# Kernel optimization log

Hardware: AMD Instinct MI355X
Metric: run time of the kernel (lower is better)

## Reference

```python
import jax, jax.numpy as jnp
import numpy as np

DT = 1e-4  # integration step, matches Model(dt=0.0001)
T = 4_000_000


def setup_inputs() -> dict:
    key = jax.random.key(0)
    ks = jax.random.split(key, 8)
    inputs = jax.random.normal(ks[0], (1, T, 3), dtype=jnp.float32)
    # time column made increasing (as in a real signal record)
    t = jnp.arange(T, dtype=jnp.float32) * DT
    inputs = inputs.at[0, :, 0].set(t)
    # small-scale 2x2 system matrices; A shifted toward -0.5*I so the
    # 4M-step linear recurrence is stable (no overflow over long horizons)
    A = -0.5 * jnp.eye(2, dtype=jnp.float32) + 0.05 * jax.random.normal(ks[1], (2, 2), jnp.float32)
    B = 0.1 * jax.random.normal(ks[2], (2, 2), jnp.float32)
    D = 0.1 * jax.random.normal(ks[3], (2, 2), jnp.float32)
    E = 0.1 * jax.random.normal(ks[4], (2, 2), jnp.float32)
    cov_in = 0.1 * jax.random.normal(ks[5], (2, 2), jnp.float32)
    training_params = jax.random.normal(ks[6], (1, 2), jnp.float32)
    initial_states = jnp.zeros((1, 5), dtype=jnp.float32)
    return {"inputs": inputs, "A": A, "B": B, "D": D, "E": E,
            "cov_in": cov_in, "training_params": training_params,
            "initial_states": initial_states}


def reference(inputs, A, B, D, E, cov_in, training_params, initial_states):
    # Faithful to GRCell.call: cov = cov_in every step (new_cov is discarded),
    # so XiCov / XiCovC / transition matrix are time-invariant constants.
    dt = jnp.float32(DT)
    sqrt2 = jnp.sqrt(jnp.float32(2.0))
    x_signal = jnp.array([1.0, 0.0], dtype=inputs.dtype)
    XiCov = (E - cov_in @ B) / sqrt2                      # (2,2)
    XiCovC = XiCov @ (-sqrt2 * B.T)                       # (2,2)
    Trans = jnp.eye(2, dtype=inputs.dtype) + (A - XiCovC) * dt  # I + (A-XiCovC)dt
    Cout = -sqrt2 * B.T * dt                              # output map, (2,2)
    p0 = training_params[0, 0]
    p1 = training_params[0, 1]
    seq = inputs[0]                                       # [T, 3] = (time, dy1, dy2)

    def step(x, inp):
        t = inp[0]
        dy = inp[1:]
        out = Cout @ x                                    # emitted BEFORE update
        x_new = Trans @ x + XiCov @ dy + (p0 * jnp.cos(p1 * t) * dt) * x_signal
        return x_new, out

    x0 = initial_states[0, :2]
    _, outs = jax.lax.scan(step, x0, seq)                 # outs: [T, 2]
    return outs[None]                                     # [1, T, 2]
```

## Files before the change

kernel.cpp:

```cpp
#include <hip/hip_runtime.h>
#include <math.h>


constexpr int   TN  = 4000000;
constexpr float FDT = 1e-4f;
constexpr int   L   = 64;
constexpr int   K   = TN / L;
constexpr int   BT  = 256;
constexpr int   NB  = (K + BT - 1) / BT;

struct Consts {
  float T00, T01, T10, T11;
  float X00, X01, X10, X11;
  float C00, C01, C10, C11;
  float p0, p1;
};

__device__ inline Consts make_consts(const float* __restrict__ A,
                                     const float* __restrict__ B,
                                     const float* __restrict__ E,
                                     const float* __restrict__ cov,
                                     const float* __restrict__ tp) {
  const float s2 = 1.41421356237309515f;
  Consts c;
  float Xi[2][2];
  for (int i = 0; i < 2; ++i)
    for (int j = 0; j < 2; ++j)
      Xi[i][j] = (E[i*2+j] - (cov[i*2+0]*B[0*2+j] + cov[i*2+1]*B[1*2+j])) / s2;
  float XiC[2][2];
  for (int i = 0; i < 2; ++i)
    for (int j = 0; j < 2; ++j)
      XiC[i][j] = Xi[i][0]*(-s2*B[j*2+0]) + Xi[i][1]*(-s2*B[j*2+1]);
  c.T00 = 1.0f + (A[0] - XiC[0][0]) * FDT;
  c.T01 =        (A[1] - XiC[0][1]) * FDT;
  c.T10 =        (A[2] - XiC[1][0]) * FDT;
  c.T11 = 1.0f + (A[3] - XiC[1][1]) * FDT;
  c.X00 = Xi[0][0]; c.X01 = Xi[0][1]; c.X10 = Xi[1][0]; c.X11 = Xi[1][1];
  c.C00 = -s2 * B[0] * FDT;
  c.C01 = -s2 * B[2] * FDT;
  c.C10 = -s2 * B[1] * FDT;
  c.C11 = -s2 * B[3] * FDT;
  c.p0 = tp[0]; c.p1 = tp[1];
  return c;
}

__device__ inline void step(float& x0, float& x1, float t, float a, float b,
                            const Consts& c) {
  float u0 = fmaf(c.X00, a, fmaf(c.X01, b, c.p0 * __cosf(c.p1 * t) * FDT));
  float u1 = fmaf(c.X10, a, c.X11 * b);
  float n0 = fmaf(c.T00, x0, fmaf(c.T01, x1, u0));
  float n1 = fmaf(c.T10, x0, fmaf(c.T11, x1, u1));
  x0 = n0; x1 = n1;
}

__device__ inline void dsq(double* M) {
  double a = M[0]*M[0] + M[1]*M[2];
  double b = M[0]*M[1] + M[1]*M[3];
  double d = M[2]*M[0] + M[3]*M[2];
  double e = M[2]*M[1] + M[3]*M[3];
  M[0] = a; M[1] = b; M[2] = d; M[3] = e;
}

__device__ inline void pow_table(const Consts& c, double (*Pw)[4], int n) {
  double M[4] = {(double)c.T00, (double)c.T01, (double)c.T10, (double)c.T11};
  for (int s = 0; s < 6; ++s) dsq(M);
  Pw[0][0] = M[0]; Pw[0][1] = M[1]; Pw[0][2] = M[2]; Pw[0][3] = M[3];
  for (int i = 1; i < n; ++i) {
    dsq(M);
    Pw[i][0] = M[0]; Pw[i][1] = M[1]; Pw[i][2] = M[2]; Pw[i][3] = M[3];
  }
}

__global__ void __launch_bounds__(BT)
k1(const float* __restrict__ seq, const float* __restrict__ A,
   const float* __restrict__ B, const float* __restrict__ E,
   const float* __restrict__ cov, const float* __restrict__ tp,
   float* __restrict__ Xe, double* __restrict__ agg) {
  const int tid  = threadIdx.x;
  const int lane = tid & 63;
  const int w    = tid >> 6;
  const int k    = blockIdx.x * BT + tid;
  Consts c = make_consts(A, B, E, cov, tp);

  float x0 = 0.f, x1 = 0.f;
  if (k < K) {
    const float4* p = (const float4*)(seq + (size_t)3 * L * k);
    #pragma unroll 4
    for (int q = 0; q < L / 4; ++q) {
      float4 fa = p[3*q+0], fb = p[3*q+1], fc = p[3*q+2];
      step(x0, x1, fa.x, fa.y, fa.z, c);
      step(x0, x1, fa.w, fb.x, fb.y, c);
      step(x0, x1, fb.z, fb.w, fc.x, c);
      step(x0, x1, fc.y, fc.z, fc.w, c);
    }
  }

  double Pw[7][4];
  pow_table(c, Pw, 7);

  double v0 = (double)x0, v1 = (double)x1;
  #pragma unroll
  for (int s = 0; s < 6; ++s) {
    int st = 1 << s;
    double p0 = __shfl_up(v0, st);
    double p1 = __shfl_up(v1, st);
    if (lane >= st) {
      double n0 = Pw[s][0]*p0 + Pw[s][1]*p1 + v0;
      double n1 = Pw[s][2]*p0 + Pw[s][3]*p1 + v1;
      v0 = n0; v1 = n1;
    }
  }

  __shared__ double wagg[4][2];
  if (lane == 63) { wagg[w][0] = v0; wagg[w][1] = v1; }
  __syncthreads();

  double E0 = 0.0, E1 = 0.0;
  for (int ww = 0; ww < w; ++ww) {
    double n0 = Pw[6][0]*E0 + Pw[6][1]*E1 + wagg[ww][0];
    double n1 = Pw[6][2]*E0 + Pw[6][3]*E1 + wagg[ww][1];
    E0 = n0; E1 = n1;
  }

  double pv0 = __shfl_up(v0, 1);
  double pv1 = __shfl_up(v1, 1);
  if (lane == 0) { pv0 = 0.0; pv1 = 0.0; }

  double M0 = 1.0, M1 = 0.0, M2 = 0.0, M3 = 1.0;
  #pragma unroll
  for (int b = 0; b < 6; ++b) {
    if ((lane >> b) & 1) {
      double a0 = Pw[b][0]*M0 + Pw[b][1]*M2;
      double a1 = Pw[b][0]*M1 + Pw[b][1]*M3;
      double a2 = Pw[b][2]*M0 + Pw[b][3]*M2;
      double a3 = Pw[b][2]*M1 + Pw[b][3]*M3;
      M0 = a0; M1 = a1; M2 = a2; M3 = a3;
    }
  }

  double e0 = M0*E0 + M1*E1 + pv0;
  double e1 = M2*E0 + M3*E1 + pv1;
  if (k < K) {
    Xe[2*k]   = (float)e0;
    Xe[2*k+1] = (float)e1;
  }
  if (tid == BT - 1) {
    agg[2*blockIdx.x]   = Pw[6][0]*E0 + Pw[6][1]*E1 + v0;
    agg[2*blockIdx.x+1] = Pw[6][2]*E0 + Pw[6][3]*E1 + v1;
  }
}

__global__ void __launch_bounds__(BT)
k2(const float* __restrict__ A, const float* __restrict__ B,
   const float* __restrict__ E, const float* __restrict__ cov,
   const float* __restrict__ tp, const float* __restrict__ ini,
   const double* __restrict__ agg, double* __restrict__ Yb) {
  __shared__ double sA[2*NB];
  __shared__ double sY[2*NB];
  for (int i = threadIdx.x; i < 2*NB; i += BT) sA[i] = agg[i];
  __syncthreads();
  if (threadIdx.x == 0) {
    Consts c = make_consts(A, B, E, cov, tp);
    double Q[4] = {(double)c.T00, (double)c.T01, (double)c.T10, (double)c.T11};
    for (int s = 0; s < 14; ++s) dsq(Q);
    double y0 = (double)ini[0], y1 = (double)ini[1];
    for (int b = 0; b < NB; ++b) {
      sY[2*b]   = y0;
      sY[2*b+1] = y1;
      double t0 = Q[0]*y0 + Q[1]*y1 + sA[2*b];
      double t1 = Q[2]*y0 + Q[3]*y1 + sA[2*b+1];
      y0 = t0; y1 = t1;
    }
  }
  __syncthreads();
  for (int i = threadIdx.x; i < 2*NB; i += BT) Yb[i] = sY[i];
}

__global__ void __launch_bounds__(BT)
k3(const float* __restrict__ seq, const float* __restrict__ A,
   const float* __restrict__ B, const float* __restrict__ E,
   const float* __restrict__ cov, const float* __restrict__ tp,
   const float* __restrict__ Xe, const double* __restrict__ Yb,
   float* __restrict__ out) {
  const int tid = threadIdx.x;
  const int k   = blockIdx.x * BT + tid;
  if (k >= K) return;
  Consts c = make_consts(A, B, E, cov, tp);

  double Pw[8][4];
  pow_table(c, Pw, 8);
  double M0 = 1.0, M1 = 0.0, M2 = 0.0, M3 = 1.0;
  #pragma unroll
  for (int b = 0; b < 8; ++b) {
    if ((tid >> b) & 1) {
      double a0 = Pw[b][0]*M0 + Pw[b][1]*M2;
      double a1 = Pw[b][0]*M1 + Pw[b][1]*M3;
      double a2 = Pw[b][2]*M0 + Pw[b][3]*M2;
      double a3 = Pw[b][2]*M1 + Pw[b][3]*M3;
      M0 = a0; M1 = a1; M2 = a2; M3 = a3;
    }
  }
  double y0 = Yb[2*blockIdx.x], y1 = Yb[2*blockIdx.x+1];
  float x0 = (float)(M0*y0 + M1*y1 + (double)Xe[2*k]);
  float x1 = (float)(M2*y0 + M3*y1 + (double)Xe[2*k+1]);

  const float4* p  = (const float4*)(seq + (size_t)3 * L * k);
  float4*       op = (float4*)(out + (size_t)2 * L * k);
  #pragma unroll 4
  for (int q = 0; q < L / 4; ++q) {
    float4 fa = p[3*q+0], fb = p[3*q+1], fc = p[3*q+2];
    float4 oA, oB;
    oA.x = fmaf(c.C00, x0, c.C01 * x1); oA.y = fmaf(c.C10, x0, c.C11 * x1);
    step(x0, x1, fa.x, fa.y, fa.z, c);
    oA.z = fmaf(c.C00, x0, c.C01 * x1); oA.w = fmaf(c.C10, x0, c.C11 * x1);
    step(x0, x1, fa.w, fb.x, fb.y, c);
    oB.x = fmaf(c.C00, x0, c.C01 * x1); oB.y = fmaf(c.C10, x0, c.C11 * x1);
    step(x0, x1, fb.z, fb.w, fc.x, c);
    oB.z = fmaf(c.C00, x0, c.C01 * x1); oB.w = fmaf(c.C10, x0, c.C11 * x1);
    step(x0, x1, fc.y, fc.z, fc.w, c);
    op[2*q]   = oA;
    op[2*q+1] = oB;
  }
}

extern "C" void kernel_launch(void* const* d_in, const int* in_sizes, int n_in,
                              void* d_out, int out_size, void* d_ws, size_t ws_size,
                              hipStream_t stream) {
  const float* seq = (const float*)d_in[0];
  const float* A   = (const float*)d_in[1];
  const float* B   = (const float*)d_in[2];
  const float* E   = (const float*)d_in[4];
  const float* cov = (const float*)d_in[5];
  const float* tp  = (const float*)d_in[6];
  const float* ini = (const float*)d_in[7];
  float* out = (float*)d_out;

  float*  Xe  = (float*)d_ws;
  double* agg = (double*)((char*)d_ws + 500224);
  double* Yb  = agg + 2 * NB;

  k1<<<NB, BT, 0, stream>>>(seq, A, B, E, cov, tp, Xe, agg);
  k2<<<1,  BT, 0, stream>>>(A, B, E, cov, tp, ini, agg, Yb);
  k3<<<NB, BT, 0, stream>>>(seq, A, B, E, cov, tp, Xe, Yb, out);
}
```

Before: 134.3 us.

## Shrink chunk length, stage input/output through LDS, parallelize block-carry scan

Cuts the per-thread chunk from 64 to 16 steps, giving four times as many threads and blocks. Input is loaded with coalesced float4 reads into padded shared memory and outputs are written back through shared memory, replacing strided per-thread global accesses. The serial single-thread carry loop over blocks in k2 is replaced by a parallel wave and block scan using matrix powers. The cost is more launched threads, more double-precision power-table setup per thread, and heavy LDS use that may limit occupancy.

Measured after the change: 127.0 us. -5.5%, faster.

```diff
diff --git a/kernel.cpp b/kernel.cpp
--- a/kernel.cpp
+++ b/kernel.cpp
@@ -2,12 +2,16 @@
 #include <math.h>
 
 
-constexpr int   TN  = 4000000;
-constexpr float FDT = 1e-4f;
-constexpr int   L   = 64;
-constexpr int   K   = TN / L;
-constexpr int   BT  = 256;
-constexpr int   NB  = (K + BT - 1) / BT;
+constexpr int   TN    = 4000000;
+constexpr float FDT   = 1e-4f;
+constexpr int   L     = 16;
+constexpr int   LOG2L = 4;
+constexpr int   K     = TN / L;
+constexpr int   BT    = 256;
+constexpr int   NB    = (K + BT - 1) / BT;
+constexpr int   ROW   = 13;
+constexpr int   F4IN  = TN * 3 / 4;
+constexpr int   F4OUT = TN * 2 / 4;
 
 struct Consts {
   float T00, T01, T10, T11;
@@ -61,9 +65,16 @@
   M[0] = a; M[1] = b; M[2] = d; M[3] = e;
 }
 
+__device__ inline void dmm(const double* a, const double* b, double* o) {
+  o[0] = a[0]*b[0] + a[1]*b[2];
+  o[1] = a[0]*b[1] + a[1]*b[3];
+  o[2] = a[2]*b[0] + a[3]*b[2];
+  o[3] = a[2]*b[1] + a[3]*b[3];
+}
+
 __device__ inline void pow_table(const Consts& c, double (*Pw)[4], int n) {
   double M[4] = {(double)c.T00, (double)c.T01, (double)c.T10, (double)c.T11};
-  for (int s = 0; s < 6; ++s) dsq(M);
+  for (int s = 0; s < LOG2L; ++s) dsq(M);
   Pw[0][0] = M[0]; Pw[0][1] = M[1]; Pw[0][2] = M[2]; Pw[0][3] = M[3];
   for (int i = 1; i < n; ++i) {
     dsq(M);
@@ -75,24 +86,37 @@
 k1(const float* __restrict__ seq, const float* __restrict__ A,
    const float* __restrict__ B, const float* __restrict__ E,
    const float* __restrict__ cov, const float* __restrict__ tp,
-   float* __restrict__ Xe, double* __restrict__ agg) {
+   float2* __restrict__ Xe, double2* __restrict__ agg) {
+  __shared__ float4  ls[BT * ROW];
+  __shared__ double  wg[4][2];
   const int tid  = threadIdx.x;
   const int lane = tid & 63;
   const int w    = tid >> 6;
   const int k    = blockIdx.x * BT + tid;
   Consts c = make_consts(A, B, E, cov, tp);
 
+  const float4* seq4 = (const float4*)seq;
+  const size_t base = (size_t)blockIdx.x * (BT * 12);
+  #pragma unroll
+  for (int i = 0; i < 12; ++i) {
+    int lf = i * BT + tid;
+    size_t f = base + (size_t)lf;
+    float4 v = make_float4(0.f, 0.f, 0.f, 0.f);
+    if (f < (size_t)F4IN) v = seq4[f];
+    int cc = lf / 12, s = lf - cc * 12;
+    ls[cc * ROW + s] = v;
+  }
+  __syncthreads();
+
   float x0 = 0.f, x1 = 0.f;
-  if (k < K) {
-    const float4* p = (const float4*)(seq + (size_t)3 * L * k);
-    #pragma unroll 4
-    for (int q = 0; q < L / 4; ++q) {
-      float4 fa = p[3*q+0], fb = p[3*q+1], fc = p[3*q+2];
-      step(x0, x1, fa.x, fa.y, fa.z, c);
-      step(x0, x1, fa.w, fb.x, fb.y, c);
-      step(x0, x1, fb.z, fb.w, fc.x, c);
-      step(x0, x1, fc.y, fc.z, fc.w, c);
-    }
+  const float4* row = &ls[tid * ROW];
+  #pragma unroll
+  for (int q = 0; q < 4; ++q) {
+    float4 fa = row[3*q], fb = row[3*q+1], fc = row[3*q+2];
+    step(x0, x1, fa.x, fa.y, fa.z, c);
+    step(x0, x1, fa.w, fb.x, fb.y, c);
+    step(x0, x1, fb.z, fb.w, fc.x, c);
+    step(x0, x1, fc.y, fc.z, fc.w, c);
   }
 
   double Pw[7][4];
@@ -110,15 +134,13 @@
       v0 = n0; v1 = n1;
     }
   }
-
-  __shared__ double wagg[4][2];
-  if (lane == 63) { wagg[w][0] = v0; wagg[w][1] = v1; }
+  if (lane == 63) { wg[w][0] = v0; wg[w][1] = v1; }
   __syncthreads();
 
   double E0 = 0.0, E1 = 0.0;
   for (int ww = 0; ww < w; ++ww) {
-    double n0 = Pw[6][0]*E0 + Pw[6][1]*E1 + wagg[ww][0];
-    double n1 = Pw[6][2]*E0 + Pw[6][3]*E1 + wagg[ww][1];
+    double n0 = Pw[6][0]*E0 + Pw[6][1]*E1 + wg[ww][0];
+    double n1 = Pw[6][2]*E0 + Pw[6][3]*E1 + wg[ww][1];
     E0 = n0; E1 = n1;
   }
 
@@ -137,16 +159,13 @@
       M0 = a0; M1 = a1; M2 = a2; M3 = a3;
     }
   }
-
   double e0 = M0*E0 + M1*E1 + pv0;
   double e1 = M2*E0 + M3*E1 + pv1;
-  if (k < K) {
-    Xe[2*k]   = (float)e0;
-    Xe[2*k+1] = (float)e1;
-  }
+  if (k < K) Xe[k] = make_float2((float)e0, (float)e1);
   if (tid == BT - 1) {
-    agg[2*blockIdx.x]   = Pw[6][0]*E0 + Pw[6][1]*E1 + v0;
-    agg[2*blockIdx.x+1] = Pw[6][2]*E0 + Pw[6][3]*E1 + v1;
+    double a0 = Pw[6][0]*E0 + Pw[6][1]*E1 + v0;
+    double a1 = Pw[6][2]*E0 + Pw[6][3]*E1 + v1;
+    agg[blockIdx.x] = make_double2(a0, a1);
   }
 }
 
@@ -154,38 +173,106 @@
 k2(const float* __restrict__ A, const float* __restrict__ B,
    const float* __restrict__ E, const float* __restrict__ cov,
    const float* __restrict__ tp, const float* __restrict__ ini,
-   const double* __restrict__ agg, double* __restrict__ Yb) {
-  __shared__ double sA[2*NB];
-  __shared__ double sY[2*NB];
-  for (int i = threadIdx.x; i < 2*NB; i += BT) sA[i] = agg[i];
-  __syncthreads();
-  if (threadIdx.x == 0) {
-    Consts c = make_consts(A, B, E, cov, tp);
-    double Q[4] = {(double)c.T00, (double)c.T01, (double)c.T10, (double)c.T11};
-    for (int s = 0; s < 14; ++s) dsq(Q);
-    double y0 = (double)ini[0], y1 = (double)ini[1];
-    for (int b = 0; b < NB; ++b) {
-      sY[2*b]   = y0;
-      sY[2*b+1] = y1;
-      double t0 = Q[0]*y0 + Q[1]*y1 + sA[2*b];
-      double t1 = Q[2]*y0 + Q[3]*y1 + sA[2*b+1];
-      y0 = t0; y1 = t1;
-    }
-  }
-  __syncthreads();
-  for (int i = threadIdx.x; i < 2*NB; i += BT) Yb[i] = sY[i];
+   const double2* __restrict__ agg, double2* __restrict__ Yb) {
+  __shared__ double wg[4][2];
+  const int tid = threadIdx.x, lane = tid & 63, w = tid >> 6;
+  Consts c = make_consts(A, B, E, cov, tp);
+
+  double Q[4] = {(double)c.T00, (double)c.T01, (double)c.T10, (double)c.T11};
+  for (int s = 0; s < LOG2L + 8; ++s) dsq(Q);
+  double Q2[4], Q3[4], Q4[4];
+  dmm(Q, Q, Q2); dmm(Q2, Q, Q3); dmm(Q2, Q2, Q4);
+  double QW[7][4];
+  for (int i = 0; i < 4; ++i) QW[0][i] = Q4[i];
+  for (int s = 1; s < 7; ++s) dmm(QW[s-1], QW[s-1], QW[s]);
+
+  double i0 = 0.0, i1 = 0.0;
+  double inc[4][2];
+  #pragma unroll
+  for (int j = 0; j < 4; ++j) {
+    int idx = 4 * tid + j;
+    double e0 = 0.0, e1 = 0.0;
+    if (idx == 0)      { e0 = (double)ini[0]; e1 = (double)ini[1]; }
+    else if (idx < NB) { double2 a = agg[idx-1]; e0 = a.x; e1 = a.y; }
+    double n0 = Q[0]*i0 + Q[1]*i1 + e0;
+    double n1 = Q[2]*i0 + Q[3]*i1 + e1;
+    i0 = n0; i1 = n1;
+    inc[j][0] = i0; inc[j][1] = i1;
+  }
+
+  double v0 = i0, v1 = i1;
+  #pragma unroll
+  for (int s = 0; s < 6; ++s) {
+    int st = 1 << s;
+    double p0 = __shfl_up(v0, st);
+    double p1 = __shfl_up(v1, st);
+    if (lane >= st) {
+      double n0 = QW[s][0]*p0 + QW[s][1]*p1 + v0;
+      double n1 = QW[s][2]*p0 + QW[s][3]*p1 + v1;
+      v0 = n0; v1 = n1;
+    }
+  }
+  if (lane == 63) { wg[w][0] = v0; wg[w][1] = v1; }
+  __syncthreads();
+  double E0 = 0.0, E1 = 0.0;
+  for (int ww = 0; ww < w; ++ww) {
+    double n0 = QW[6][0]*E0 + QW[6][1]*E1 + wg[ww][0];
+    double n1 = QW[6][2]*E0 + QW[6][3]*E1 + wg[ww][1];
+    E0 = n0; E1 = n1;
+  }
+  double pv0 = __shfl_up(v0, 1);
+  double pv1 = __shfl_up(v1, 1);
+  if (lane == 0) { pv0 = 0.0; pv1 = 0.0; }
+
+  double M0 = 1.0, M1 = 0.0, M2 = 0.0, M3 = 1.0;
+  #pragma unroll
+  for (int b = 0; b < 6; ++b) {
+    if ((lane >> b) & 1) {
+      double a0 = QW[b][0]*M0 + QW[b][1]*M2;
+      double a1 = QW[b][0]*M1 + QW[b][1]*M3;
+      double a2 = QW[b][2]*M0 + QW[b][3]*M2;
+      double a3 = QW[b][2]*M1 + QW[b][3]*M3;
+      M0 = a0; M1 = a1; M2 = a2; M3 = a3;
+    }
+  }
+  double Eth0 = M0*E0 + M1*E1 + pv0;
+  double Eth1 = M2*E0 + M3*E1 + pv1;
+
+  const double* Pj[4] = {Q, Q2, Q3, Q4};
+  #pragma unroll
+  for (int j = 0; j < 4; ++j) {
+    int idx = 4 * tid + j;
+    if (idx < NB) {
+      double y0 = Pj[j][0]*Eth0 + Pj[j][1]*Eth1 + inc[j][0];
+      double y1 = Pj[j][2]*Eth0 + Pj[j][3]*Eth1 + inc[j][1];
+      Yb[idx] = make_double2(y0, y1);
+    }
+  }
 }
 
 __global__ void __launch_bounds__(BT)
 k3(const float* __restrict__ seq, const float* __restrict__ A,
    const float* __restrict__ B, const float* __restrict__ E,
    const float* __restrict__ cov, const float* __restrict__ tp,
-   const float* __restrict__ Xe, const double* __restrict__ Yb,
+   const float2* __restrict__ Xe, const double2* __restrict__ Yb,
    float* __restrict__ out) {
+  __shared__ float4 ls[BT * ROW];
   const int tid = threadIdx.x;
   const int k   = blockIdx.x * BT + tid;
-  if (k >= K) return;
   Consts c = make_consts(A, B, E, cov, tp);
+
+  const float4* seq4 = (const float4*)seq;
+  const size_t base = (size_t)blockIdx.x * (BT * 12);
+  #pragma unroll
+  for (int i = 0; i < 12; ++i) {
+    int lf = i * BT + tid;
+    size_t f = base + (size_t)lf;
+    float4 v = make_float4(0.f, 0.f, 0.f, 0.f);
+    if (f < (size_t)F4IN) v = seq4[f];
+    int cc = lf / 12, s = lf - cc * 12;
+    ls[cc * ROW + s] = v;
+  }
+  __syncthreads();
 
   double Pw[8][4];
   pow_table(c, Pw, 8);
@@ -200,15 +287,15 @@
       M0 = a0; M1 = a1; M2 = a2; M3 = a3;
     }
   }
-  double y0 = Yb[2*blockIdx.x], y1 = Yb[2*blockIdx.x+1];
-  float x0 = (float)(M0*y0 + M1*y1 + (double)Xe[2*k]);
-  float x1 = (float)(M2*y0 + M3*y1 + (double)Xe[2*k+1]);
-
-  const float4* p  = (const float4*)(seq + (size_t)3 * L * k);
-  float4*       op = (float4*)(out + (size_t)2 * L * k);
-  #pragma unroll 4
-  for (int q = 0; q < L / 4; ++q) {
-    float4 fa = p[3*q+0], fb = p[3*q+1], fc = p[3*q+2];
+  double2 yb = Yb[blockIdx.x];
+  float2 xe = (k < K) ? Xe[k] : make_float2(0.f, 0.f);
+  float x0 = (float)(M0*yb.x + M1*yb.y + (double)xe.x);
+  float x1 = (float)(M2*yb.x + M3*yb.y + (double)xe.y);
+
+  float4* row = &ls[tid * ROW];
+  #pragma unroll
+  for (int q = 0; q < 4; ++q) {
+    float4 fa = row[3*q], fb = row[3*q+1], fc = row[3*q+2];
     float4 oA, oB;
     oA.x = fmaf(c.C00, x0, c.C01 * x1); oA.y = fmaf(c.C10, x0, c.C11 * x1);
     step(x0, x1, fa.x, fa.y, fa.z, c);
@@ -218,8 +305,21 @@
     step(x0, x1, fb.z, fb.w, fc.x, c);
     oB.z = fmaf(c.C00, x0, c.C01 * x1); oB.w = fmaf(c.C10, x0, c.C11 * x1);
     step(x0, x1, fc.y, fc.z, fc.w, c);
-    op[2*q]   = oA;
-    op[2*q+1] = oB;
+    row[2*q]   = oA;
+    row[2*q+1] = oB;
+  }
+  __syncthreads();
+
+  float4* out4 = (float4*)out;
+  const size_t obase = (size_t)blockIdx.x * (BT * 8);
+  #pragma unroll
+  for (int i = 0; i < 8; ++i) {
+    int lf = i * BT + tid;
+    size_t g = obase + (size_t)lf;
+    if (g < (size_t)F4OUT) {
+      int cc = lf >> 3, s = lf & 7;
+      out4[g] = ls[cc * ROW + s];
+    }
   }
 }
 
@@ -235,9 +335,9 @@
   const float* ini = (const float*)d_in[7];
   float* out = (float*)d_out;
 
-  float*  Xe  = (float*)d_ws;
-  double* agg = (double*)((char*)d_ws + 500224);
-  double* Yb  = agg + 2 * NB;
+  float2*  Xe  = (float2*)d_ws;
+  double2* agg = (double2*)((char*)d_ws + 2000000);
+  double2* Yb  = (double2*)((char*)d_ws + 2000000 + 16384);
 
   k1<<<NB, BT, 0, stream>>>(seq, A, B, E, cov, tp, Xe, agg);
   k2<<<1,  BT, 0, stream>>>(A, B, E, cov, tp, ini, agg, Yb);
```
